# Optimization experiments

Hardware: AMD Instinct MI355X
Metric: run time of the kernel (lower is better)

## Reference

```python
import jax, jax.numpy as jnp
import numpy as np

GRID = 64
NPTS = 2048
EPS = 1e-5


def gridding_reverse(grid3):
    # grid3: [B,S,S,S] occupancy grid -> point cloud [B,S^3,3] in [-1,1];
    # each vertex is the weight-averaged position of its 8 adjacent cells, zero if empty.
    B, S = grid3.shape[0], grid3.shape[1]
    g = jnp.pad(grid3, ((0, 0), (1, 0), (1, 0), (1, 0)))
    ax = jnp.arange(S, dtype=grid3.dtype)
    cx, cy, cz = jnp.meshgrid(ax, ax, ax, indexing='ij')
    base = jnp.stack([cx, cy, cz], axis=-1)  # [S,S,S,3]
    wsum = jnp.zeros((B, S, S, S), grid3.dtype)
    pos = jnp.zeros((B, S, S, S, 3), grid3.dtype)
    for dx in (0, 1):
        for dy in (0, 1):
            for dz in (0, 1):
                w = g[:, dx:dx + S, dy:dy + S, dz:dz + S]
                off = jnp.asarray([dx - 1.0, dy - 1.0, dz - 1.0], grid3.dtype)
                pos = pos + w[..., None] * (base + off)
                wsum = wsum + w
    avg = pos / jnp.maximum(wsum, 1e-8)[..., None]
    pt = avg / (S * 0.5) - 1.0
    pt = jnp.where((wsum > 0)[..., None], pt, 0.0)
    return pt.reshape(B, S * S * S, 3)


def maxpool3d(x, k):
    return jax.lax.reduce_window(x, -jnp.inf, jax.lax.max, (1, 1, k, k, k), (1, 1, k, k, k), 'VALID')


def random_point_sampling(cloud, noise, n_points):
    # uniformly pick n_points among points with nonzero coord-sum (random-score top-k
    # replaces torch.randperm per sample; fixed output shape, jit-safe)
    mask = jnp.sum(cloud, axis=2) != 0
    scores = jnp.where(mask, noise, -1e30)
    idx = jax.lax.top_k(scores, n_points)[1]  # [B,n_points]
    return jnp.take_along_axis(cloud, idx[..., None], axis=1)


def cubic_feature_sampling(pt, feat):
    # pt [B,N,3] in [-1,1]; feat [B,C,S,S,S] -> [B,N,8*C]: features at the 8 corners
    # of the cell containing each point.
    B, C, S = feat.shape[0], feat.shape[1], feat.shape[2]
    featf = jnp.transpose(feat.reshape(B, C, S * S * S), (0, 2, 1))  # [B,S^3,C]
    lo = jnp.floor((pt + 1.0) * (0.5 * S)).astype(jnp.int32)  # lower corner index
    outs = []
    for dx in (0, 1):
        for dy in (0, 1):
            for dz in (0, 1):
                ix = jnp.clip(lo[..., 0] + dx, 0, S - 1)
                iy = jnp.clip(lo[..., 1] + dy, 0, S - 1)
                iz = jnp.clip(lo[..., 2] + dz, 0, S - 1)
                lin = (ix * S + iy) * S + iz  # [B,N]
                outs.append(jnp.take_along_axis(featf, lin[..., None], axis=1))
    return jnp.concatenate(outs, axis=-1)  # [B,N,8C]


def conv1d(x, w, b):
    y = jax.lax.conv_general_dilated(x, w, (1,), [(1, 1)], dimension_numbers=('NCH', 'OIH', 'NCH'))
    return y + b[None, :, None]


def bn1d(x, g, b, m, v):
    inv = jax.lax.rsqrt(v + EPS) * g
    return x * inv[None, :, None] + (b - m * inv)[None, :, None]


def setup_inputs():
    key = jax.random.key(0)
    ks = jax.random.split(key, 32)
    B = 8

    def nrm(k, shape, fan):
        return (jax.random.normal(k, shape, jnp.float32) / np.sqrt(fan)).astype(jnp.float32)

    inp = {
        'data': jax.random.normal(ks[0], (B, 1, GRID, GRID, GRID), jnp.float32),
        'skip_32': jax.random.normal(ks[1], (B, 32, 32, 32, 32), jnp.float32),
        'skip_16': jax.random.normal(ks[2], (B, 64, 16, 16, 16), jnp.float32),
        'skip_8': jax.random.normal(ks[3], (B, 128, 8, 8, 8), jnp.float32),
        'noise': jax.random.normal(ks[4], (B, 4096), jnp.float32),
        'w11': nrm(ks[5], (1792, 1792), 1792), 'b11': jnp.zeros(1792, jnp.float32),
        'w12': nrm(ks[6], (1792, 448), 1792), 'b12': jnp.zeros(448, jnp.float32),
        'w13': nrm(ks[7], (448, 100), 448), 'b13': jnp.zeros(100, jnp.float32),
        'c1w': nrm(ks[8], (1024, 2048, 3), 2048 * 3), 'c1b': jnp.zeros(1024, jnp.float32),
        'g1': jnp.ones(1024, jnp.float32), 'be1': jnp.zeros(1024, jnp.float32),
        'm1': 0.01 * jax.random.normal(ks[9], (1024,), jnp.float32),
        'v1': 1.0 + 0.1 * jax.random.uniform(ks[10], (1024,), jnp.float32),
        'c2w': nrm(ks[11], (512, 1024, 3), 1024 * 3), 'c2b': jnp.zeros(512, jnp.float32),
        'g2': jnp.ones(512, jnp.float32), 'be2': jnp.zeros(512, jnp.float32),
        'm2': 0.01 * jax.random.normal(ks[12], (512,), jnp.float32),
        'v2': 1.0 + 0.1 * jax.random.uniform(ks[13], (512,), jnp.float32),
        'c3w': nrm(ks[14], (128, 512, 3), 512 * 3), 'c3b': jnp.zeros(128, jnp.float32),
        'g3': jnp.ones(128, jnp.float32), 'be3': jnp.zeros(128, jnp.float32),
        'm3': 0.01 * jax.random.normal(ks[15], (128,), jnp.float32),
        'v3': 1.0 + 0.1 * jax.random.uniform(ks[16], (128,), jnp.float32),
        'c4w': nrm(ks[17], (32, 128, 3), 128 * 3), 'c4b': jnp.zeros(32, jnp.float32),
        'g4': jnp.ones(32, jnp.float32), 'be4': jnp.zeros(32, jnp.float32),
        'm4': 0.01 * jax.random.normal(ks[18], (32,), jnp.float32),
        'v4': 1.0 + 0.1 * jax.random.uniform(ks[19], (32,), jnp.float32),
        'w15a': nrm(ks[20], (3200, 512), 3200), 'b15a': jnp.zeros(512, jnp.float32),
        'w15b': nrm(ks[21], (512, 128), 512), 'b15b': jnp.zeros(128, jnp.float32),
        'w15c': nrm(ks[22], (128, 15), 128), 'b15c': jnp.zeros(15, jnp.float32),
    }
    return inp


def reference(data, skip_32, skip_16, skip_8, noise,
              w11, b11, w12, b12, w13, b13,
              c1w, c1b, g1, be1, m1, v1,
              c2w, c2b, g2, be2, m2, v2,
              c3w, c3b, g3, be3, m3, v3,
              c4w, c4b, g4, be4, m4, v4,
              w15a, b15a, w15b, b15b, w15c, b15c):
    B = data.shape[0]
    completion = (jnp.abs(data) <= 1.0).astype(jnp.float32)  # [B,1,64,64,64]
    pt = gridding_reverse(completion[:, 0])                  # [B,64^3,3]
    x = pt.reshape(B, 3, GRID, GRID, GRID)                   # raw reshape as in source
    x = maxpool3d(x, 4)                                      # [B,3,16,16,16]
    cloud = x.reshape(B, 4096, 3)
    cloud = random_point_sampling(cloud, noise, NPTS)        # [B,2048,3]
    f = jnp.concatenate([
        cubic_feature_sampling(cloud, skip_32),              # [B,2048,256]
        cubic_feature_sampling(cloud, skip_16),              # [B,2048,512]
        cubic_feature_sampling(cloud, skip_8)], axis=2)      # [B,2048,1792]
    f = jax.nn.relu(f @ w11 + b11)
    f = jax.nn.relu(f @ w12 + b12)
    f = jax.nn.relu(f @ w13 + b13)                           # [B,2048,100]
    y = jax.nn.relu(bn1d(conv1d(f, c1w, c1b), g1, be1, m1, v1))
    y = jax.nn.relu(bn1d(conv1d(y, c2w, c2b), g2, be2, m2, v2))
    y = jax.nn.relu(bn1d(conv1d(y, c3w, c3b), g3, be3, m3, v3))
    y = jax.nn.relu(bn1d(conv1d(y, c4w, c4b), g4, be4, m4, v4))  # [B,32,100]
    h = y.reshape(B, -1)                                     # [B,3200]
    h = jax.nn.relu(h @ w15a + b15a)                         # dropout = identity (eval)
    h = jax.nn.relu(h @ w15b + b15b)
    return h @ w15c + b15c                                   # [B,15]
```

## Files before the change

kernel.cpp:

```cpp
#include <hip/hip_runtime.h>
#include <cstdint>

#define S64 64
#define S3 (S64*S64*S64)
#define NB 8
#define NPTS 2048

typedef unsigned short ushort_t;
typedef __attribute__((ext_vector_type(8))) short bh8;
typedef __attribute__((ext_vector_type(4))) float f4v;

__device__ inline ushort_t bf_rne(float a) {
    unsigned u = __float_as_uint(a);
    unsigned r = (u + 0x7FFFu + ((u >> 16) & 1u)) >> 16;
    return (ushort_t)r;
}
__device__ inline void split2(float a, ushort_t& h, ushort_t& lo) {
    h = bf_rne(a);
    float hf = __uint_as_float(((unsigned)h) << 16);
    lo = bf_rne(a - hf);
}

__global__ void k_gridding(const float* __restrict__ data, float* __restrict__ pt_buf) {
    int idx = blockIdx.x * blockDim.x + threadIdx.x;
    if (idx >= NB * S3) return;
    int b = idx / S3;
    int cell = idx - b * S3;
    int i = cell >> 12;
    int j = (cell >> 6) & 63;
    int k = cell & 63;
    const float* db = data + (size_t)b * S3;
    float wsum = 0.f, px = 0.f, py = 0.f, pz = 0.f;
#pragma unroll
    for (int dx = 0; dx < 2; ++dx)
#pragma unroll
    for (int dy = 0; dy < 2; ++dy)
#pragma unroll
    for (int dz = 0; dz < 2; ++dz) {
        int xi = i + dx - 1, yj = j + dy - 1, zk = k + dz - 1;
        float w = 0.f;
        if (xi >= 0 && yj >= 0 && zk >= 0) {
            float v = db[((xi << 6) + yj << 6) + zk];
            w = (fabsf(v) <= 1.0f) ? 1.0f : 0.0f;
        }
        px += w * (float)xi;
        py += w * (float)yj;
        pz += w * (float)zk;
        wsum += w;
    }
    float wc = fmaxf(wsum, 1e-8f);
    float ptx = (px / wc) / 32.0f - 1.0f;
    float pty = (py / wc) / 32.0f - 1.0f;
    float ptz = (pz / wc) / 32.0f - 1.0f;
    if (!(wsum > 0.f)) { ptx = 0.f; pty = 0.f; ptz = 0.f; }
    float* o = pt_buf + (size_t)b * (S3 * 3) + (size_t)cell * 3;
    o[0] = ptx; o[1] = pty; o[2] = ptz;
}

__global__ void k_maxpool(const float* __restrict__ pt_buf, float* __restrict__ pooled) {
    int idx = blockIdx.x * blockDim.x + threadIdx.x;
    if (idx >= NB * 12288) return;
    int b = idx / 12288;
    int r = idx - b * 12288;
    int c = r >> 12;
    int r2 = r & 4095;
    int X = r2 >> 8;
    int Y = (r2 >> 4) & 15;
    int Z = r2 & 15;
    const float* src = pt_buf + (size_t)b * (S3 * 3) + (size_t)c * S3;
    float m = -INFINITY;
#pragma unroll
    for (int u = 0; u < 4; ++u)
#pragma unroll
    for (int v = 0; v < 4; ++v)
#pragma unroll
    for (int w = 0; w < 4; ++w) {
        float val = src[((4 * X + u) << 12) + ((4 * Y + v) << 6) + (4 * Z + w)];
        m = fmaxf(m, val);
    }
    pooled[idx] = m;
}

__global__ void k_topk(const float* __restrict__ pooled, const float* __restrict__ noise,
                       float* __restrict__ sc) {
    __shared__ unsigned long long keys[4096];
    int b = blockIdx.x;
    int tid = threadIdx.x;
    for (int p = tid; p < 4096; p += 1024) {
        const float* cp = pooled + (size_t)b * 12288 + (size_t)p * 3;
        float ssum = (cp[0] + cp[1]) + cp[2];
        float score = (ssum != 0.0f) ? noise[b * 4096 + p] : -1e30f;
        unsigned int u = __float_as_uint(score);
        unsigned int s = (u & 0x80000000u) ? ~u : (u | 0x80000000u);
        keys[p] = ((unsigned long long)(~s) << 32) | (unsigned int)p;
    }
    __syncthreads();
    for (int k = 2; k <= 4096; k <<= 1) {
        for (int j = k >> 1; j > 0; j >>= 1) {
            for (int t = tid; t < 4096; t += 1024) {
                int ixj = t ^ j;
                if (ixj > t) {
                    bool up = ((t & k) == 0);
                    unsigned long long a = keys[t], c = keys[ixj];
                    if (up ? (a > c) : (a < c)) { keys[t] = c; keys[ixj] = a; }
                }
            }
            __syncthreads();
        }
    }
    for (int r = tid; r < NPTS; r += 1024) {
        int p = (int)(keys[r] & 0xFFFFFFFFu);
        const float* cp = pooled + (size_t)b * 12288 + (size_t)p * 3;
        float* o = sc + ((size_t)b * NPTS + r) * 3;
        o[0] = cp[0]; o[1] = cp[1]; o[2] = cp[2];
    }
}

__global__ void k_cubic(const float* __restrict__ sc,
                        const float* __restrict__ s32,
                        const float* __restrict__ s16,
                        const float* __restrict__ s8,
                        ushort_t* __restrict__ Ap, int row0) {
    int rl = blockIdx.y;
    int row = row0 + rl;
    int col = blockIdx.x * 256 + threadIdx.x;
    int b = row >> 11;
    const float* p = sc + (size_t)row * 3;
    float ptx = p[0], pty = p[1], ptz = p[2];
    const float* feat;
    int S, c, q;
    if (col < 256)      { S = 32; q = col >> 5;  c = col & 31;
                          feat = s32 + (size_t)b * 32 * 32768; }
    else if (col < 768) { int cc = col - 256; S = 16; q = cc >> 6; c = cc & 63;
                          feat = s16 + (size_t)b * 64 * 4096; }
    else                { int cc = col - 768; S = 8;  q = cc >> 7; c = cc & 127;
                          feat = s8 + (size_t)b * 128 * 512; }
    int dx = (q >> 2) & 1, dy = (q >> 1) & 1, dz = q & 1;
    float half = 0.5f * (float)S;
    int lx = (int)floorf((ptx + 1.0f) * half);
    int ly = (int)floorf((pty + 1.0f) * half);
    int lz = (int)floorf((ptz + 1.0f) * half);
    int ix = min(max(lx + dx, 0), S - 1);
    int iy = min(max(ly + dy, 0), S - 1);
    int iz = min(max(lz + dz, 0), S - 1);
    int lin = (ix * S + iy) * S + iz;
    float v = feat[(size_t)c * S * S * S + lin];
    ushort_t h, lo; split2(v, h, lo);
    size_t base = (size_t)rl * 5376 + 3 * (size_t)col;
    Ap[base] = h; Ap[base + 1] = h; Ap[base + 2] = lo;
}

__global__ void k_split_transpose(const float* __restrict__ W, ushort_t* __restrict__ Bp,
                                  int K, int N, int Npad) {
    __shared__ float t[32][33];
    int tx = threadIdx.x, ty = threadIdx.y;
    int n0 = blockIdx.x * 32, k0 = blockIdx.y * 32;
#pragma unroll
    for (int kk = 0; kk < 4; ++kk) {
        int k = k0 + ty + kk * 8, n = n0 + tx;
        float v = (k < K && n < N) ? W[(size_t)k * N + n] : 0.f;
        t[ty + kk * 8][tx] = v;
    }
    __syncthreads();
    size_t Kp = 3 * (size_t)K;
#pragma unroll
    for (int nn = 0; nn < 4; ++nn) {
        int n = n0 + ty + nn * 8;
        int k = k0 + tx;
        if (n >= Npad || k >= K) continue;
        float a = t[tx][ty + nn * 8];
        ushort_t h, lo; split2(a, h, lo);
        size_t base = (size_t)n * Kp + 3 * (size_t)k;
        Bp[base] = h; Bp[base + 1] = lo; Bp[base + 2] = h;
    }
}

__global__ void k_split_rows_b(const float* __restrict__ src, ushort_t* __restrict__ dst, int K) {
    int r = blockIdx.y;
    int k = blockIdx.x * 256 + threadIdx.x;
    if (k >= K) return;
    float a = src[(size_t)r * K + k];
    ushort_t h, lo; split2(a, h, lo);
    size_t base = (size_t)r * (3 * (size_t)K) + 3 * (size_t)k;
    dst[base] = h; dst[base + 1] = lo; dst[base + 2] = h;
}

__global__ void k_split_im2col(const float* __restrict__ src, ushort_t* __restrict__ Ap,
                               int Cin, int Kin) {
    int mp = blockIdx.y;
    int k = blockIdx.x * 256 + threadIdx.x;
    if (k >= Kin) return;
    float v = 0.f;
    if (mp < 800) {
        int b = mp / 100, h = mp - b * 100;
        int c = k / 3, t = k - c * 3;
        int hh = h + t - 1;
        if (hh >= 0 && hh < 100)
            v = src[((size_t)b * Cin + c) * 100 + hh];
    }
    ushort_t h16, lo; split2(v, h16, lo);
    size_t base = (size_t)mp * (3 * (size_t)Kin) + 3 * (size_t)k;
    Ap[base] = h16; Ap[base + 1] = h16; Ap[base + 2] = lo;
}

__global__ void k_zero(float* __restrict__ p, int n) {
    int i = blockIdx.x * 256 + threadIdx.x;
    if (i < n) p[i] = 0.f;
}

__global__ void k_epi(const float* __restrict__ acc, const float* __restrict__ bias,
                      const float* __restrict__ bn_g, const float* __restrict__ bn_b,
                      const float* __restrict__ bn_m, const float* __restrict__ bn_v,
                      float* __restrict__ Cf, ushort_t* __restrict__ Cs,
                      int M, int N, int ldc, int relu, int dobn, int mode) {
    int idx = blockIdx.x * 256 + threadIdx.x;
    if (idx >= M * N) return;
    int m = idx / N, n = idx - m * N;
    float v = acc[idx] + bias[n];
    if (dobn) {
        float inv = rsqrtf(bn_v[n] + 1e-5f) * bn_g[n];
        v = v * inv + (bn_b[n] - bn_m[n] * inv);
    }
    if (relu) v = fmaxf(v, 0.f);
    if (mode == 0) {
        Cf[idx] = v;
    } else if (mode == 1) {
        int b = m / 100, h = m - b * 100;
        Cf[((size_t)b * N + n) * 100 + h] = v;
    } else {
        ushort_t h, lo; split2(v, h, lo);
        size_t base = (size_t)m * ldc + 3 * (size_t)n;
        Cs[base] = h; Cs[base + 1] = h; Cs[base + 2] = lo;
    }
}

#define GLDS(g, s) __builtin_amdgcn_global_load_lds( \
    (const __attribute__((address_space(1))) void*)(g), \
    (__attribute__((address_space(3))) void*)(s), 16, 0, 0)

__global__ __launch_bounds__(256) void k_gemm_mfma(
    const ushort_t* __restrict__ Ap, const ushort_t* __restrict__ Bp,
    const float* __restrict__ bias,
    const float* __restrict__ bn_g, const float* __restrict__ bn_b,
    const float* __restrict__ bn_m, const float* __restrict__ bn_v,
    float* __restrict__ Cf, ushort_t* __restrict__ Cs,
    int M, int N, int Kp, int ldc,
    int relu, int dobn, int omode, int osplit,
    int ks, int Kc)
{
    __shared__ short As[2][128][32];
    __shared__ short Bs[2][128][32];
    int tid = threadIdx.x;
    int l = tid & 63, w = tid >> 6;
    int wr = w >> 1, wc = w & 1;
    int m0 = blockIdx.y * 128, n0 = blockIdx.x * 128;
    int kbeg = blockIdx.z * Kc;

    f4v acc[4][4];
#pragma unroll
    for (int i = 0; i < 4; ++i)
#pragma unroll
        for (int j = 0; j < 4; ++j) acc[i][j] = (f4v){0.f, 0.f, 0.f, 0.f};

    int lr = l >> 2;
    int lc = l & 3;
    const ushort_t* pa0 = Ap + (size_t)(m0 + w * 32 + lr) * Kp + lc * 8 + kbeg;
    const ushort_t* pa1 = pa0 + (size_t)16 * Kp;
    const ushort_t* pb0 = Bp + (size_t)(n0 + w * 32 + lr) * Kp + lc * 8 + kbeg;
    const ushort_t* pb1 = pb0 + (size_t)16 * Kp;

    int ko = (l >> 4) * 8;
    int fr = l & 15;
    int nt = Kc >> 5;

    GLDS(pa0, &As[0][w * 32][0]);
    GLDS(pa1, &As[0][w * 32 + 16][0]);
    GLDS(pb0, &Bs[0][w * 32][0]);
    GLDS(pb1, &Bs[0][w * 32 + 16][0]);
    __syncthreads();

    for (int t = 0; t < nt; ++t) {
        int cur = t & 1;
        if (t + 1 < nt) {
            int ko2 = (t + 1) << 5;
            GLDS(pa0 + ko2, &As[cur ^ 1][w * 32][0]);
            GLDS(pa1 + ko2, &As[cur ^ 1][w * 32 + 16][0]);
            GLDS(pb0 + ko2, &Bs[cur ^ 1][w * 32][0]);
            GLDS(pb1 + ko2, &Bs[cur ^ 1][w * 32 + 16][0]);
        }
        bh8 af[4], bfr[4];
#pragma unroll
        for (int i = 0; i < 4; ++i)
            af[i] = *reinterpret_cast<const bh8*>(&As[cur][wr * 64 + i * 16 + fr][ko]);
#pragma unroll
        for (int j = 0; j < 4; ++j)
            bfr[j] = *reinterpret_cast<const bh8*>(&Bs[cur][wc * 64 + j * 16 + fr][ko]);
#pragma unroll
        for (int i = 0; i < 4; ++i)
#pragma unroll
            for (int j = 0; j < 4; ++j)
                acc[i][j] = __builtin_amdgcn_mfma_f32_16x16x32_bf16(af[i], bfr[j], acc[i][j], 0, 0, 0);
        __syncthreads();
    }

#pragma unroll
    for (int i = 0; i < 4; ++i)
#pragma unroll
        for (int j = 0; j < 4; ++j) {
#pragma unroll
            for (int r = 0; r < 4; ++r) {
                int m = m0 + wr * 64 + i * 16 + (l >> 4) * 4 + r;
                int n = n0 + wc * 64 + j * 16 + fr;
                if (m >= M || n >= N) continue;
                if (ks > 1) {
                    atomicAdd(&Cf[(size_t)m * N + n], acc[i][j][r]);
                    continue;
                }
                float v = acc[i][j][r] + bias[n];
                if (dobn) {
                    float inv = rsqrtf(bn_v[n] + 1e-5f) * bn_g[n];
                    v = v * inv + (bn_b[n] - bn_m[n] * inv);
                }
                if (relu) v = fmaxf(v, 0.f);
                if (osplit) {
                    ushort_t h, lo; split2(v, h, lo);
                    size_t base = (size_t)m * ldc + 3 * (size_t)n;
                    Cs[base] = h; Cs[base + 1] = h; Cs[base + 2] = lo;
                } else if (omode == 0) {
                    Cf[(size_t)m * N + n] = v;
                } else {
                    int bb = m / 100, h = m - bb * 100;
                    Cf[((size_t)bb * N + n) * 100 + h] = v;
                }
            }
        }
}

__global__ __launch_bounds__(256) void k_skinny(
    const float* __restrict__ A, const float* __restrict__ B,
    const float* __restrict__ bias, float* __restrict__ C,
    int M, int N, int K, int relu)
{
    int n = blockIdx.x * 64 + (threadIdx.x & 63);
    int m = blockIdx.y * 4 + (threadIdx.x >> 6);
    if (m >= M || n >= N) return;
    const float* a = A + (size_t)m * K;
    const float* b = B + n;
    float acc = 0.f;
    int k = 0;
#pragma unroll 4
    for (; k + 4 <= K; k += 4) {
        acc = fmaf(a[k],     b[(size_t)k * N],       acc);
        acc = fmaf(a[k + 1], b[(size_t)(k + 1) * N], acc);
        acc = fmaf(a[k + 2], b[(size_t)(k + 2) * N], acc);
        acc = fmaf(a[k + 3], b[(size_t)(k + 3) * N], acc);
    }
    for (; k < K; ++k) acc = fmaf(a[k], b[(size_t)k * N], acc);
    float v = acc + bias[n];
    if (relu) v = fmaxf(v, 0.f);
    C[(size_t)m * N + n] = v;
}

extern "C" void kernel_launch(void* const* d_in, const int* in_sizes, int n_in,
                              void* d_out, int out_size, void* d_ws, size_t ws_size,
                              hipStream_t stream) {
    const float* data  = (const float*)d_in[0];
    const float* s32   = (const float*)d_in[1];
    const float* s16   = (const float*)d_in[2];
    const float* s8    = (const float*)d_in[3];
    const float* noise = (const float*)d_in[4];
    const float* w11 = (const float*)d_in[5];  const float* b11 = (const float*)d_in[6];
    const float* w12 = (const float*)d_in[7];  const float* b12 = (const float*)d_in[8];
    const float* w13 = (const float*)d_in[9];  const float* b13 = (const float*)d_in[10];
    const float* c1w = (const float*)d_in[11]; const float* c1b = (const float*)d_in[12];
    const float* g1 = (const float*)d_in[13];  const float* be1 = (const float*)d_in[14];
    const float* m1 = (const float*)d_in[15];  const float* v1  = (const float*)d_in[16];
    const float* c2w = (const float*)d_in[17]; const float* c2b = (const float*)d_in[18];
    const float* g2 = (const float*)d_in[19];  const float* be2 = (const float*)d_in[20];
    const float* m2 = (const float*)d_in[21];  const float* v2  = (const float*)d_in[22];
    const float* c3w = (const float*)d_in[23]; const float* c3b = (const float*)d_in[24];
    const float* g3 = (const float*)d_in[25];  const float* be3 = (const float*)d_in[26];
    const float* m3 = (const float*)d_in[27];  const float* v3  = (const float*)d_in[28];
    const float* c4w = (const float*)d_in[29]; const float* c4b = (const float*)d_in[30];
    const float* g4 = (const float*)d_in[31];  const float* be4 = (const float*)d_in[32];
    const float* m4 = (const float*)d_in[33];  const float* v4  = (const float*)d_in[34];
    const float* w15a = (const float*)d_in[35]; const float* b15a = (const float*)d_in[36];
    const float* w15b = (const float*)d_in[37]; const float* b15b = (const float*)d_in[38];
    const float* w15c = (const float*)d_in[39]; const float* b15c = (const float*)d_in[40];
    float* out = (float*)d_out;
    (void)in_sizes; (void)n_in; (void)out_size; (void)ws_size;

    char* ws = (char*)d_ws;
    size_t off = 0;
    auto alloc = [&](size_t bytes) { size_t o = off; off += (bytes + 255) & ~(size_t)255; return o; };

    size_t rA  = alloc((size_t)4096 * 5376 * 2);
    size_t rF  = alloc((size_t)4096 * 5376 * 2);
    size_t rG  = alloc((size_t)4096 * 1344 * 2);
    size_t rW1 = alloc((size_t)1792 * 5376 * 2);
    size_t rW2 = alloc((size_t)512  * 5376 * 2);
    size_t rW3 = alloc((size_t)128  * 1344 * 2);
    size_t rAcc = alloc((size_t)4096 * 448 * 4);
    size_t o_f4 = alloc((size_t)16384 * 100 * 4);
    size_t o_y1 = alloc((size_t)NB * 1024 * 100 * 4);
    size_t o_y2 = alloc((size_t)NB * 512 * 100 * 4);
    size_t o_y3 = alloc((size_t)NB * 128 * 100 * 4);
    size_t o_y4 = alloc((size_t)NB * 32 * 100 * 4);
    size_t o_pooled = alloc(NB * 12288 * 4);
    size_t o_sc     = alloc(NB * NPTS * 3 * 4);
    size_t o_h2     = alloc(NB * 512 * 4);
    size_t o_h3     = alloc(NB * 128 * 4);

    float*    pt_buf = (float*)(ws + rA);
    ushort_t* Aq     = (ushort_t*)(ws + rA);
    ushort_t* Aconv  = (ushort_t*)(ws + rA);
    ushort_t* Fq     = (ushort_t*)(ws + rF);
    ushort_t* Bconv  = (ushort_t*)(ws + rF);
    ushort_t* Gq     = (ushort_t*)(ws + rG);
    ushort_t* Bp1    = (ushort_t*)(ws + rW1);
    ushort_t* Bp2    = (ushort_t*)(ws + rW2);
    ushort_t* Bp3    = (ushort_t*)(ws + rW3);
    float*    Cacc   = (float*)(ws + rAcc);
    float* f4     = (float*)(ws + o_f4);
    float* y1     = (float*)(ws + o_y1);
    float* y2     = (float*)(ws + o_y2);
    float* y3     = (float*)(ws + o_y3);
    float* y4     = (float*)(ws + o_y4);
    float* pooled = (float*)(ws + o_pooled);
    float* scb    = (float*)(ws + o_sc);
    float* h2     = (float*)(ws + o_h2);
    float* h3     = (float*)(ws + o_h3);

    k_gridding<<<(NB * S3 + 255) / 256, 256, 0, stream>>>(data, pt_buf);
    k_maxpool<<<(NB * 12288 + 255) / 256, 256, 0, stream>>>(pt_buf, pooled);
    k_topk<<<NB, 1024, 0, stream>>>(pooled, noise, scb);

    k_split_transpose<<<dim3(56, 56), dim3(32, 8), 0, stream>>>(w11, Bp1, 1792, 1792, 1792);
    k_split_transpose<<<dim3(16, 56), dim3(32, 8), 0, stream>>>(w12, Bp2, 1792, 448, 512);
    k_split_transpose<<<dim3(4, 14),  dim3(32, 8), 0, stream>>>(w13, Bp3, 448, 100, 128);

    for (int q = 0; q < 4; ++q) {
        k_cubic<<<dim3(7, 4096), 256, 0, stream>>>(scb, s32, s16, s8, Aq, q * 4096);
        k_gemm_mfma<<<dim3(14, 32), 256, 0, stream>>>(Aq, Bp1, b11,
            nullptr, nullptr, nullptr, nullptr, nullptr, Fq,
            4096, 1792, 5376, 5376, 1, 0, 0, 1, 1, 5376);
        k_zero<<<(4096 * 448 + 255) / 256, 256, 0, stream>>>(Cacc, 4096 * 448);
        k_gemm_mfma<<<dim3(4, 32, 4), 256, 0, stream>>>(Fq, Bp2, nullptr,
            nullptr, nullptr, nullptr, nullptr, Cacc, nullptr,
            4096, 448, 5376, 0, 0, 0, 0, 0, 4, 1344);
        k_epi<<<(4096 * 448 + 255) / 256, 256, 0, stream>>>(Cacc, b12,
            nullptr, nullptr, nullptr, nullptr, nullptr, Gq,
            4096, 448, 1344, 1, 0, 2);
        k_zero<<<(4096 * 100 + 255) / 256, 256, 0, stream>>>(Cacc, 4096 * 100);
        k_gemm_mfma<<<dim3(1, 32, 6), 256, 0, stream>>>(Gq, Bp3, nullptr,
            nullptr, nullptr, nullptr, nullptr, Cacc, nullptr,
            4096, 100, 1344, 0, 0, 0, 0, 0, 6, 224);
        k_epi<<<(4096 * 100 + 255) / 256, 256, 0, stream>>>(Cacc, b13,
            nullptr, nullptr, nullptr, nullptr, f4 + (size_t)q * 4096 * 100, nullptr,
            4096, 100, 0, 1, 0, 0);
    }

    k_split_im2col<<<dim3(24, 896), 256, 0, stream>>>(f4, Aconv, 2048, 6144);
    k_split_rows_b<<<dim3(24, 1024), 256, 0, stream>>>(c1w, Bconv, 6144);
    k_zero<<<(800 * 1024 + 255) / 256, 256, 0, stream>>>(Cacc, 800 * 1024);
    k_gemm_mfma<<<dim3(8, 7, 8), 256, 0, stream>>>(Aconv, Bconv, nullptr,
        nullptr, nullptr, nullptr, nullptr, Cacc, nullptr,
        800, 1024, 18432, 0, 0, 0, 0, 0, 8, 2304);
    k_epi<<<(800 * 1024 + 255) / 256, 256, 0, stream>>>(Cacc, c1b,
        g1, be1, m1, v1, y1, nullptr, 800, 1024, 0, 1, 1, 1);

    k_split_im2col<<<dim3(12, 896), 256, 0, stream>>>(y1, Aconv, 1024, 3072);
    k_split_rows_b<<<dim3(12, 512), 256, 0, stream>>>(c2w, Bconv, 3072);
    k_zero<<<(800 * 512 + 255) / 256, 256, 0, stream>>>(Cacc, 800 * 512);
    k_gemm_mfma<<<dim3(4, 7, 8), 256, 0, stream>>>(Aconv, Bconv, nullptr,
        nullptr, nullptr, nullptr, nullptr, Cacc, nullptr,
        800, 512, 9216, 0, 0, 0, 0, 0, 8, 1152);
    k_epi<<<(800 * 512 + 255) / 256, 256, 0, stream>>>(Cacc, c2b,
        g2, be2, m2, v2, y2, nullptr, 800, 512, 0, 1, 1, 1);

    k_split_im2col<<<dim3(6, 896), 256, 0, stream>>>(y2, Aconv, 512, 1536);
    k_split_rows_b<<<dim3(6, 128), 256, 0, stream>>>(c3w, Bconv, 1536);
    k_zero<<<(800 * 128 + 255) / 256, 256, 0, stream>>>(Cacc, 800 * 128);
    k_gemm_mfma<<<dim3(1, 7, 16), 256, 0, stream>>>(Aconv, Bconv, nullptr,
        nullptr, nullptr, nullptr, nullptr, Cacc, nullptr,
        800, 128, 4608, 0, 0, 0, 0, 0, 16, 288);
    k_epi<<<(800 * 128 + 255) / 256, 256, 0, stream>>>(Cacc, c3b,
        g3, be3, m3, v3, y3, nullptr, 800, 128, 0, 1, 1, 1);

    k_split_im2col<<<dim3(2, 896), 256, 0, stream>>>(y3, Aconv, 128, 384);
    k_split_rows_b<<<dim3(2, 32), 256, 0, stream>>>(c4w, Bconv, 384);
    k_zero<<<(800 * 32 + 255) / 256, 256, 0, stream>>>(Cacc, 800 * 32);
    k_gemm_mfma<<<dim3(1, 7, 6), 256, 0, stream>>>(Aconv, Bconv, nullptr,
        nullptr, nullptr, nullptr, nullptr, Cacc, nullptr,
        800, 32, 1152, 0, 0, 0, 0, 0, 6, 192);
    k_epi<<<(800 * 32 + 255) / 256, 256, 0, stream>>>(Cacc, c4b,
        g4, be4, m4, v4, y4, nullptr, 800, 32, 0, 1, 1, 1);

    k_skinny<<<dim3(8, 2), 256, 0, stream>>>(y4, w15a, b15a, h2, 8, 512, 3200, 1);
    k_skinny<<<dim3(2, 2), 256, 0, stream>>>(h2, w15b, b15b, h3, 8, 128, 512, 1);
    k_skinny<<<dim3(1, 2), 256, 0, stream>>>(h3, w15c, b15c, out, 8, 15, 128, 0);
}
```

Baseline: 1.666 ms.

## Swizzle GEMM LDS layout, unroll skinny GEMV, and enlarge FC batch partitions

Three separate changes. The MFMA GEMM now XOR-swizzles the 8-element column chunk by row group, on both the global-to-LDS copy and the fragment reads, to cut LDS bank conflicts. The skinny GEMV unrolls its inner loop by 8 instead of 4. The FC stage now sizes its workspace at runtime and processes 8192 points per partition when the workspace fits (otherwise 4096), halving the launch count and using less split-K for FC2. In exchange the FC stage needs more workspace, and the swizzle must match exactly between the write and read sides.

```diff
diff --git a/kernel.cpp b/kernel.cpp
--- a/kernel.cpp
+++ b/kernel.cpp
@@ -264,13 +264,14 @@
 
     int lr = l >> 2;
     int lc = l & 3;
-    const ushort_t* pa0 = Ap + (size_t)(m0 + w * 32 + lr) * Kp + lc * 8 + kbeg;
+    int lcs = lc ^ ((lr >> 2) & 3);
+    const ushort_t* pa0 = Ap + (size_t)(m0 + w * 32 + lr) * Kp + lcs * 8 + kbeg;
     const ushort_t* pa1 = pa0 + (size_t)16 * Kp;
-    const ushort_t* pb0 = Bp + (size_t)(n0 + w * 32 + lr) * Kp + lc * 8 + kbeg;
+    const ushort_t* pb0 = Bp + (size_t)(n0 + w * 32 + lr) * Kp + lcs * 8 + kbeg;
     const ushort_t* pb1 = pb0 + (size_t)16 * Kp;
 
-    int ko = (l >> 4) * 8;
     int fr = l & 15;
+    int ko = ((l >> 4) ^ ((fr >> 2) & 3)) * 8;
     int nt = Kc >> 5;
 
     GLDS(pa0, &As[0][w * 32][0]);
@@ -348,12 +349,11 @@
     const float* b = B + n;
     float acc = 0.f;
     int k = 0;
-#pragma unroll 4
-    for (; k + 4 <= K; k += 4) {
-        acc = fmaf(a[k],     b[(size_t)k * N],       acc);
-        acc = fmaf(a[k + 1], b[(size_t)(k + 1) * N], acc);
-        acc = fmaf(a[k + 2], b[(size_t)(k + 2) * N], acc);
-        acc = fmaf(a[k + 3], b[(size_t)(k + 3) * N], acc);
+#pragma unroll 8
+    for (; k + 8 <= K; k += 8) {
+#pragma unroll
+        for (int u = 0; u < 8; ++u)
+            acc = fmaf(a[k + u], b[(size_t)(k + u) * N], acc);
     }
     for (; k < K; ++k) acc = fmaf(a[k], b[(size_t)k * N], acc);
     float v = acc + bias[n];
@@ -388,48 +388,59 @@
     const float* w15b = (const float*)d_in[37]; const float* b15b = (const float*)d_in[38];
     const float* w15c = (const float*)d_in[39]; const float* b15c = (const float*)d_in[40];
     float* out = (float*)d_out;
-    (void)in_sizes; (void)n_in; (void)out_size; (void)ws_size;
+    (void)in_sizes; (void)n_in; (void)out_size;
 
     char* ws = (char*)d_ws;
-    size_t off = 0;
-    auto alloc = [&](size_t bytes) { size_t o = off; off += (bytes + 255) & ~(size_t)255; return o; };
-
-    size_t rA  = alloc((size_t)4096 * 5376 * 2);
-    size_t rF  = alloc((size_t)4096 * 5376 * 2);
-    size_t rG  = alloc((size_t)4096 * 1344 * 2);
-    size_t rW1 = alloc((size_t)1792 * 5376 * 2);
-    size_t rW2 = alloc((size_t)512  * 5376 * 2);
-    size_t rW3 = alloc((size_t)128  * 1344 * 2);
-    size_t rAcc = alloc((size_t)4096 * 448 * 4);
-    size_t o_f4 = alloc((size_t)16384 * 100 * 4);
-    size_t o_y1 = alloc((size_t)NB * 1024 * 100 * 4);
-    size_t o_y2 = alloc((size_t)NB * 512 * 100 * 4);
-    size_t o_y3 = alloc((size_t)NB * 128 * 100 * 4);
-    size_t o_y4 = alloc((size_t)NB * 32 * 100 * 4);
-    size_t o_pooled = alloc(NB * 12288 * 4);
-    size_t o_sc     = alloc(NB * NPTS * 3 * 4);
-    size_t o_h2     = alloc(NB * 512 * 4);
-    size_t o_h3     = alloc(NB * 128 * 4);
-
-    float*    pt_buf = (float*)(ws + rA);
-    ushort_t* Aq     = (ushort_t*)(ws + rA);
-    ushort_t* Aconv  = (ushort_t*)(ws + rA);
-    ushort_t* Fq     = (ushort_t*)(ws + rF);
-    ushort_t* Bconv  = (ushort_t*)(ws + rF);
-    ushort_t* Gq     = (ushort_t*)(ws + rG);
-    ushort_t* Bp1    = (ushort_t*)(ws + rW1);
-    ushort_t* Bp2    = (ushort_t*)(ws + rW2);
-    ushort_t* Bp3    = (ushort_t*)(ws + rW3);
-    float*    Cacc   = (float*)(ws + rAcc);
-    float* f4     = (float*)(ws + o_f4);
-    float* y1     = (float*)(ws + o_y1);
-    float* y2     = (float*)(ws + o_y2);
-    float* y3     = (float*)(ws + o_y3);
-    float* y4     = (float*)(ws + o_y4);
-    float* pooled = (float*)(ws + o_pooled);
-    float* scb    = (float*)(ws + o_sc);
-    float* h2     = (float*)(ws + o_h2);
-    float* h3     = (float*)(ws + o_h3);
+
+    size_t offs[16];
+    auto plan = [&](size_t P, size_t* o) -> size_t {
+        size_t off = 0;
+        auto al = [&](size_t b) { size_t x = off; off += (b + 255) & ~(size_t)255; return x; };
+        o[0]  = al(P * 5376 * 2);
+        o[1]  = al(P * 5376 * 2);
+        o[2]  = al(P * 1344 * 2);
+        o[3]  = al((size_t)1792 * 5376 * 2);
+        o[4]  = al((size_t)512 * 5376 * 2);
+        o[5]  = al((size_t)128 * 1344 * 2);
+        o[6]  = al(P * 448 * 4);
+        o[7]  = al((size_t)16384 * 100 * 4);
+        o[8]  = al((size_t)NB * 1024 * 100 * 4);
+        o[9]  = al((size_t)NB * 512 * 100 * 4);
+        o[10] = al((size_t)NB * 128 * 100 * 4);
+        o[11] = al((size_t)NB * 32 * 100 * 4);
+        o[12] = al(NB * 12288 * 4);
+        o[13] = al(NB * NPTS * 3 * 4);
+        o[14] = al(NB * 512 * 4);
+        o[15] = al(NB * 128 * 4);
+        return off;
+    };
+    size_t P = 8192;
+    if (plan(P, offs) > ws_size) P = 4096;
+    plan(P, offs);
+    int nparts = (int)(16384 / P);
+    int Pb = (int)(P / 128);
+    int ksFC2 = (P == 8192) ? 2 : 4;
+    int KcFC2 = 5376 / ksFC2;
+
+    float*    pt_buf = (float*)(ws + offs[0]);
+    ushort_t* Aq     = (ushort_t*)(ws + offs[0]);
+    ushort_t* Aconv  = (ushort_t*)(ws + offs[0]);
+    ushort_t* Fq     = (ushort_t*)(ws + offs[1]);
+    ushort_t* Bconv  = (ushort_t*)(ws + offs[1]);
+    ushort_t* Gq     = (ushort_t*)(ws + offs[2]);
+    ushort_t* Bp1    = (ushort_t*)(ws + offs[3]);
+    ushort_t* Bp2    = (ushort_t*)(ws + offs[4]);
+    ushort_t* Bp3    = (ushort_t*)(ws + offs[5]);
+    float*    Cacc   = (float*)(ws + offs[6]);
+    float* f4     = (float*)(ws + offs[7]);
+    float* y1     = (float*)(ws + offs[8]);
+    float* y2     = (float*)(ws + offs[9]);
+    float* y3     = (float*)(ws + offs[10]);
+    float* y4     = (float*)(ws + offs[11]);
+    float* pooled = (float*)(ws + offs[12]);
+    float* scb    = (float*)(ws + offs[13]);
+    float* h2     = (float*)(ws + offs[14]);
+    float* h3     = (float*)(ws + offs[15]);
 
     k_gridding<<<(NB * S3 + 255) / 256, 256, 0, stream>>>(data, pt_buf);
     k_maxpool<<<(NB * 12288 + 255) / 256, 256, 0, stream>>>(pt_buf, pooled);
@@ -439,25 +450,25 @@
     k_split_transpose<<<dim3(16, 56), dim3(32, 8), 0, stream>>>(w12, Bp2, 1792, 448, 512);
     k_split_transpose<<<dim3(4, 14),  dim3(32, 8), 0, stream>>>(w13, Bp3, 448, 100, 128);
 
-    for (int q = 0; q < 4; ++q) {
-        k_cubic<<<dim3(7, 4096), 256, 0, stream>>>(scb, s32, s16, s8, Aq, q * 4096);
-        k_gemm_mfma<<<dim3(14, 32), 256, 0, stream>>>(Aq, Bp1, b11,
+    for (int q = 0; q < nparts; ++q) {
+        k_cubic<<<dim3(7, (unsigned)P), 256, 0, stream>>>(scb, s32, s16, s8, Aq, q * (int)P);
+        k_gemm_mfma<<<dim3(14, Pb), 256, 0, stream>>>(Aq, Bp1, b11,
             nullptr, nullptr, nullptr, nullptr, nullptr, Fq,
-            4096, 1792, 5376, 5376, 1, 0, 0, 1, 1, 5376);
-        k_zero<<<(4096 * 448 + 255) / 256, 256, 0, stream>>>(Cacc, 4096 * 448);
-        k_gemm_mfma<<<dim3(4, 32, 4), 256, 0, stream>>>(Fq, Bp2, nullptr,
+            (int)P, 1792, 5376, 5376, 1, 0, 0, 1, 1, 5376);
+        k_zero<<<((int)P * 448 + 255) / 256, 256, 0, stream>>>(Cacc, (int)P * 448);
+        k_gemm_mfma<<<dim3(4, Pb, ksFC2), 256, 0, stream>>>(Fq, Bp2, nullptr,
             nullptr, nullptr, nullptr, nullptr, Cacc, nullptr,
-            4096, 448, 5376, 0, 0, 0, 0, 0, 4, 1344);
-        k_epi<<<(4096 * 448 + 255) / 256, 256, 0, stream>>>(Cacc, b12,
+            (int)P, 448, 5376, 0, 0, 0, 0, 0, ksFC2, KcFC2);
+        k_epi<<<((int)P * 448 + 255) / 256, 256, 0, stream>>>(Cacc, b12,
             nullptr, nullptr, nullptr, nullptr, nullptr, Gq,
-            4096, 448, 1344, 1, 0, 2);
-        k_zero<<<(4096 * 100 + 255) / 256, 256, 0, stream>>>(Cacc, 4096 * 100);
-        k_gemm_mfma<<<dim3(1, 32, 6), 256, 0, stream>>>(Gq, Bp3, nullptr,
+            (int)P, 448, 1344, 1, 0, 2);
+        k_zero<<<((int)P * 100 + 255) / 256, 256, 0, stream>>>(Cacc, (int)P * 100);
+        k_gemm_mfma<<<dim3(1, Pb, 6), 256, 0, stream>>>(Gq, Bp3, nullptr,
             nullptr, nullptr, nullptr, nullptr, Cacc, nullptr,
-            4096, 100, 1344, 0, 0, 0, 0, 0, 6, 224);
-        k_epi<<<(4096 * 100 + 255) / 256, 256, 0, stream>>>(Cacc, b13,
-            nullptr, nullptr, nullptr, nullptr, f4 + (size_t)q * 4096 * 100, nullptr,
-            4096, 100, 0, 1, 0, 0);
+            (int)P, 100, 1344, 0, 0, 0, 0, 0, 6, 224);
+        k_epi<<<((int)P * 100 + 255) / 256, 256, 0, stream>>>(Cacc, b13,
+            nullptr, nullptr, nullptr, nullptr, f4 + (size_t)q * P * 100, nullptr,
+            (int)P, 100, 0, 1, 0, 0);
     }
 
     k_split_im2col<<<dim3(24, 896), 256, 0, stream>>>(f4, Aconv, 2048, 6144);
```

Measured after the change: 2.784 ms. 67.1% more time.
